# Kernel tuning notes

Hardware: AMD Instinct MI355X
Metric: run time of the kernel (lower is better)

## Reference

```python
import jax, jax.numpy as jnp
import numpy as np

B, T, D = 4, 2048, 1024
H = 16
HD = D // H  # 64
MAX_POS = 4096


def setup_inputs() -> dict:
    key = jax.random.key(0)
    k1, k2, k3, k4 = jax.random.split(key, 4)
    x = jax.random.normal(k1, (B, T, D), dtype=jnp.float32)
    position_ids = jnp.sort(jax.random.randint(k2, (B, T), 0, MAX_POS), axis=-1)
    Wqkv = jax.random.normal(k3, (D, 3 * D), dtype=jnp.float32) * (D ** -0.5)
    Wout = jax.random.normal(k4, (D, D), dtype=jnp.float32) * (D ** -0.5)
    return {"x": x, "position_ids": position_ids, "Wqkv": Wqkv, "Wout": Wout}


def reference(x, position_ids, Wqkv, Wout):
    Bv, Tv, Dv = x.shape
    # qkv projection: (B,T,3,H,HD)
    qkv = (x @ Wqkv).reshape(Bv, Tv, 3, H, HD)
    q, k, v = jnp.moveaxis(qkv, 2, 0)  # each (B,T,H,HD)
    q = q.transpose(0, 2, 1, 3)  # (B,H,T,HD)
    k = k.transpose(0, 2, 1, 3)
    v = v.transpose(0, 2, 1, 3)
    scale = 1.0 / jnp.sqrt(jnp.asarray(HD, dtype=x.dtype))
    attn = jnp.einsum('bhid,bhjd->bhij', q, k) * scale  # (B,H,T,T)
    # position-derived causal mask: attend only where pos_i >= pos_j
    causal_mask = position_ids[:, None, :, None] < position_ids[:, None, None, :]
    attn = jnp.where(causal_mask, -jnp.inf, attn)
    attn = jax.nn.softmax(attn, axis=-1)
    attn = jnp.nan_to_num(attn, nan=0.0)
    out = jnp.einsum('bhij,bhjd->bhid', attn, v)  # (B,H,T,HD)
    out = out.transpose(0, 2, 1, 3).reshape(Bv, Tv, Dv)
    return out @ Wout
```

## Files before the change

### kernel.cpp

```cpp
#include <hip/hip_runtime.h>
#include <math.h>

#define NB 4
#define NT 2048
#define ND 1024
#define NH 16
#define NHD 64
#define N3D 3072
#define M1 8192

typedef __attribute__((ext_vector_type(8))) short bf16x8;
typedef __attribute__((ext_vector_type(4))) float f32x4;
typedef __attribute__((ext_vector_type(16))) float f32x16;
typedef __attribute__((ext_vector_type(2))) int i32x2;
typedef unsigned short u16;
typedef unsigned int u32;

__device__ __forceinline__ u32 bf16rn(float f) {
    u32 u = __float_as_uint(f);
    return (u + 0x7FFFu + ((u >> 16) & 1u)) >> 16;
}
__device__ __forceinline__ u32 pack2(float a, float b) {
    return bf16rn(a) | (bf16rn(b) << 16);
}
__device__ __forceinline__ u32 cvtpk(float lo, float hi) {
    u32 r;
    asm("v_cvt_pk_bf16_f32 %0, %1, %2" : "=v"(r) : "v"(lo), "v"(hi));
    return r;
}
__device__ __forceinline__ void pswap(u32& a, u32& b) {
    i32x2 r = __builtin_amdgcn_permlane32_swap((int)a, (int)b, false, false);
    a = (u32)r.x; b = (u32)r.y;
}

__global__ __launch_bounds__(256) void convx_kernel(const float* __restrict__ in, u16* __restrict__ out) {
    const int idx = blockIdx.x * 256 + threadIdx.x;
    const float4 v = *reinterpret_cast<const float4*>(in + (size_t)idx * 4);
    *reinterpret_cast<uint2*>(out + (size_t)idx * 4) = make_uint2(pack2(v.x, v.y), pack2(v.z, v.w));
}

__global__ __launch_bounds__(256) void tconv_kernel(const float* __restrict__ in, u16* __restrict__ out,
                                                    int R, int C) {
    __shared__ float t[32][33];
    const int bx = blockIdx.x * 32, by = blockIdx.y * 32;
    const int x = threadIdx.x, y0 = threadIdx.y;
    #pragma unroll
    for (int yy = y0; yy < 32; yy += 8) t[yy][x] = in[(size_t)(by + yy) * C + bx + x];
    __syncthreads();
    #pragma unroll
    for (int yy = y0; yy < 32; yy += 8) out[(size_t)(bx + yy) * R + by + x] = (u16)bf16rn(t[x][yy]);
}

#define GEMM_PROLOGUE(Aptr, Btptr)                                                            \
    __shared__ __align__(16) u16 As[4096];                                                    \
    __shared__ __align__(16) u16 Bs[4096];                                                    \
    const int tid = threadIdx.x;                                                              \
    const int lane = tid & 63, wave = tid >> 6;                                               \
    const int wr = wave >> 1, wc = wave & 1;                                                  \
    const int n0 = blockIdx.x * 128, m0 = blockIdx.y * 128;                                   \
    const int c0 = tid, c1 = tid + 256;                                                      \
    const int pA0 = (c0 * 16) ^ ((((c0 * 16) >> 6) & 7) << 4);                                \
    const int pA1 = (c1 * 16) ^ ((((c1 * 16) >> 6) & 7) << 4);                                \
    const u16* gA0 = Aptr + (size_t)(m0 + (c0 >> 2)) * 1024 + (c0 & 3) * 8;                   \
    const u16* gA1 = Aptr + (size_t)(m0 + (c1 >> 2)) * 1024 + (c1 & 3) * 8;                   \
    const u16* gB0 = Btptr + (size_t)(n0 + (c0 >> 2)) * 1024 + (c0 & 3) * 8;                  \
    const u16* gB1 = Btptr + (size_t)(n0 + (c1 >> 2)) * 1024 + (c1 & 3) * 8;                  \
    int offA[4], offB[4];                                                                     \
    {                                                                                         \
        const int kb = (lane >> 4) * 16;                                                      \
        _Pragma("unroll")                                                                     \
        for (int mm = 0; mm < 4; ++mm) {                                                      \
            int row = wr * 64 + mm * 16 + (lane & 15);                                        \
            offA[mm] = (row * 64 + kb) ^ ((row & 7) << 4);                                    \
        }                                                                                     \
        _Pragma("unroll")                                                                     \
        for (int nn = 0; nn < 4; ++nn) {                                                      \
            int row = wc * 64 + nn * 16 + (lane & 15);                                        \
            offB[nn] = (row * 64 + kb) ^ ((row & 7) << 4);                                    \
        }                                                                                     \
    }                                                                                         \
    f32x4 acc[4][4];                                                                          \
    _Pragma("unroll")                                                                         \
    for (int mm = 0; mm < 4; ++mm)                                                            \
        _Pragma("unroll")                                                                     \
        for (int nn = 0; nn < 4; ++nn)                                                        \
            acc[mm][nn] = (f32x4){0.f, 0.f, 0.f, 0.f};                                        \
    uint4 va0 = *(const uint4*)gA0, va1 = *(const uint4*)gA1;                                 \
    uint4 vb0 = *(const uint4*)gB0, vb1 = *(const uint4*)gB1;                                 \
    for (int k0 = 0; k0 < 1024; k0 += 32) {                                                   \
        __syncthreads();                                                                      \
        *(uint4*)((char*)As + pA0) = va0;                                                     \
        *(uint4*)((char*)As + pA1) = va1;                                                     \
        *(uint4*)((char*)Bs + pA0) = vb0;                                                     \
        *(uint4*)((char*)Bs + pA1) = vb1;                                                     \
        __syncthreads();                                                                      \
        if (k0 + 32 < 1024) {                                                                 \
            gA0 += 32; gA1 += 32; gB0 += 32; gB1 += 32;                                       \
            va0 = *(const uint4*)gA0; va1 = *(const uint4*)gA1;                               \
            vb0 = *(const uint4*)gB0; vb1 = *(const uint4*)gB1;                               \
        }                                                                                     \
        bf16x8 aF[4], bF[4];                                                                  \
        _Pragma("unroll")                                                                     \
        for (int mm = 0; mm < 4; ++mm) aF[mm] = *(const bf16x8*)((const char*)As + offA[mm]); \
        _Pragma("unroll")                                                                     \
        for (int nn = 0; nn < 4; ++nn) bF[nn] = *(const bf16x8*)((const char*)Bs + offB[nn]); \
        _Pragma("unroll")                                                                     \
        for (int mm = 0; mm < 4; ++mm)                                                        \
            _Pragma("unroll")                                                                 \
            for (int nn = 0; nn < 4; ++nn)                                                    \
                acc[mm][nn] = __builtin_amdgcn_mfma_f32_16x16x32_bf16(bF[nn], aF[mm],         \
                                                                      acc[mm][nn], 0, 0, 0); \
    }

__global__ __launch_bounds__(256) void gemm_qkv_kernel(
    const u16* __restrict__ A, const u16* __restrict__ Bt,
    u16* __restrict__ Qo, u16* __restrict__ Ko, u16* __restrict__ Vo)
{
    GEMM_PROLOGUE(A, Bt)
    const float qsc = 0.18033688011112042f;
    const int col16 = lane & 15, g4 = (lane >> 4) << 2;
    const int nb0 = n0 + wc * 64;
    const int tb0 = m0 + wr * 64;
    const int s = nb0 >> 10;
    if (s == 0) {
        #pragma unroll
        for (int mm = 0; mm < 4; ++mm) {
            const int t = tb0 + mm * 16 + col16;
            const int bq = t >> 11, tt = t & 2047;
            #pragma unroll
            for (int nn = 0; nn < 4; ++nn) {
                const int n_abs = nb0 + nn * 16 + g4;
                const int hh = (n_abs >> 6) & 15, hd = n_abs & 63;
                uint2 w = make_uint2(pack2(acc[mm][nn][0] * qsc, acc[mm][nn][1] * qsc),
                                     pack2(acc[mm][nn][2] * qsc, acc[mm][nn][3] * qsc));
                *reinterpret_cast<uint2*>(&Qo[((size_t)((bq << 4) + hh) * 2048 + tt) * 64 + hd]) = w;
            }
        }
    } else if (s == 1) {
        #pragma unroll
        for (int mm = 0; mm < 4; ++mm) {
            const int t = tb0 + mm * 16 + col16;
            const int bq = t >> 11, tt = t & 2047;
            #pragma unroll
            for (int nn = 0; nn < 4; ++nn) {
                const int n_abs = nb0 + nn * 16 + g4;
                const int hh = (n_abs >> 6) & 15, hd = n_abs & 63;
                uint2 w = make_uint2(pack2(acc[mm][nn][0], acc[mm][nn][1]),
                                     pack2(acc[mm][nn][2], acc[mm][nn][3]));
                *reinterpret_cast<uint2*>(&Ko[((size_t)((bq << 4) + hh) * 2048 + tt) * 64 + hd]) = w;
            }
        }
    } else {
        #pragma unroll
        for (int mm = 0; mm < 4; ++mm) {
            const int t = tb0 + mm * 16 + col16;
            const int bq = t >> 11, tt = t & 2047;
            #pragma unroll
            for (int nn = 0; nn < 4; ++nn) {
                const int n_abs = nb0 + nn * 16 + g4;
                const int hh = (n_abs >> 6) & 15, hd = n_abs & 63;
                const size_t vbase = ((size_t)((bq << 4) + hh) * 64 + hd) * 2048 + tt;
                #pragma unroll
                for (int r = 0; r < 4; ++r)
                    Vo[vbase + (size_t)r * 2048] = (u16)bf16rn(acc[mm][nn][r]);
            }
        }
    }
}

__global__ __launch_bounds__(256) void gemm_out_kernel(
    const u16* __restrict__ A, const u16* __restrict__ Bt, float* __restrict__ C)
{
    GEMM_PROLOGUE(A, Bt)
    const int col16 = lane & 15, g4 = (lane >> 4) << 2;
    #pragma unroll
    for (int mm = 0; mm < 4; ++mm) {
        const int m = m0 + wr * 64 + mm * 16 + col16;
        #pragma unroll
        for (int nn = 0; nn < 4; ++nn) {
            const int n_a = n0 + wc * 64 + nn * 16 + g4;
            *reinterpret_cast<float4*>(&C[(size_t)m * 1024 + n_a]) =
                make_float4(acc[mm][nn][0], acc[mm][nn][1], acc[mm][nn][2], acc[mm][nn][3]);
        }
    }
}

__global__ __launch_bounds__(64) void attn5_kernel(
    const u16* __restrict__ Q, const u16* __restrict__ K, const u16* __restrict__ Vt,
    const int* __restrict__ pos, u16* __restrict__ AO)
{
    const int bid = blockIdx.x;
    const int wg  = ((bid & 7) << 9) + (bid >> 3);
    const int bh  = wg >> 6;
    const int qw  = 63 - (wg & 63);
    const int b = bh >> 4, h = bh & 15;
    const int lane = threadIdx.x;
    const int col = lane & 31, hi = lane >> 5;
    const int i0 = qw * 32;

    int bnd;
    {
        const int target = pos[b * 2048 + i0 + col];
        int lo = 0, hic = 2048;
        #pragma unroll
        for (int it = 0; it < 12; ++it) {
            const int mid = (lo + hic) >> 1;
            if (lo < hic) { if (pos[b * 2048 + mid] <= target) lo = mid + 1; else hic = mid; }
        }
        bnd = lo;
    }
    int bmax = bnd, bmin = bnd;
    #pragma unroll
    for (int s = 1; s < 32; s <<= 1) {
        bmax = max(bmax, __shfl_xor(bmax, s));
        bmin = min(bmin, __shfl_xor(bmin, s));
    }

    const size_t kvrow = (size_t)bh * 2048;
    const size_t vrow  = (size_t)bh * 64;

    bf16x8 qf[4];
    #pragma unroll
    for (int ds = 0; ds < 4; ++ds)
        qf[ds] = *(const bf16x8*)&Q[(kvrow + i0 + col) * 64 + ds * 16 + hi * 8];

    const int hi4 = 4 * hi;

    float mrun = -INFINITY, lrun = 0.f;
    f32x16 oT0, oT1;
    #pragma unroll
    for (int i = 0; i < 16; ++i) { oT0[i] = 0.f; oT1[i] = 0.f; }

    for (int j0 = 0; j0 < bmax; j0 += 32) {
        bf16x8 kf[4], vfa[2], vfb[2];
        #pragma unroll
        for (int ds = 0; ds < 4; ++ds)
            kf[ds] = *(const bf16x8*)&K[(kvrow + j0 + col) * 64 + ds * 16 + hi * 8];
        #pragma unroll
        for (int kh = 0; kh < 2; ++kh) {
            vfa[kh] = *(const bf16x8*)&Vt[(vrow + col) * 2048 + j0 + kh * 16 + hi * 8];
            vfb[kh] = *(const bf16x8*)&Vt[(vrow + 32 + col) * 2048 + j0 + kh * 16 + hi * 8];
        }

        f32x16 st;
        #pragma unroll
        for (int i = 0; i < 16; ++i) st[i] = 0.f;
        #pragma unroll
        for (int ds = 0; ds < 4; ++ds)
            st = __builtin_amdgcn_mfma_f32_32x32x16_bf16(kf[ds], qf[ds], st, 0, 0, 0);

        if (j0 + 32 > bmin) {
            #pragma unroll
            for (int r = 0; r < 16; ++r) {
                const int kg = j0 + ((r & 3) + 8 * (r >> 2)) + hi4;
                if (kg >= bnd) st[r] = -INFINITY;
            }
        }

        float rm = st[0];
        #pragma unroll
        for (int r = 1; r < 16; ++r) rm = fmaxf(rm, st[r]);
        rm = fmaxf(rm, __shfl_xor(rm, 32));
        if (__any(rm > mrun)) {
            const float mnew = fmaxf(mrun, rm);
            const float factor = __builtin_amdgcn_exp2f(mrun - mnew);
            mrun = mnew;
            lrun *= factor;
            #pragma unroll
            for (int i = 0; i < 16; ++i) { oT0[i] *= factor; oT1[i] *= factor; }
        }
        float psum = 0.f;
        #pragma unroll
        for (int r = 0; r < 16; ++r) {
            const float p = __builtin_amdgcn_exp2f(st[r] - mrun);
            st[r] = p;
            psum += p;
        }
        psum += __shfl_xor(psum, 32);
        lrun += psum;

        u32 W[8];
        #pragma unroll
        for (int r = 0; r < 8; ++r) W[r] = cvtpk(st[2 * r], st[2 * r + 1]);

        u32 a0 = W[0], b0 = W[2]; pswap(a0, b0);
        u32 a1 = W[1], b1 = W[3]; pswap(a1, b1);
        u32 a2 = W[4], b2 = W[6]; pswap(a2, b2);
        u32 a3 = W[5], b3 = W[7]; pswap(a3, b3);
        union { u32 w[4]; bf16x8 v; } p0, p1;
        p0.w[0] = a0; p0.w[1] = a1; p0.w[2] = b0; p0.w[3] = b1;
        p1.w[0] = a2; p1.w[1] = a3; p1.w[2] = b2; p1.w[3] = b3;

        oT0 = __builtin_amdgcn_mfma_f32_32x32x16_bf16(vfa[0], p0.v, oT0, 0, 0, 0);
        oT0 = __builtin_amdgcn_mfma_f32_32x32x16_bf16(vfa[1], p1.v, oT0, 0, 0, 0);
        oT1 = __builtin_amdgcn_mfma_f32_32x32x16_bf16(vfb[0], p0.v, oT1, 0, 0, 0);
        oT1 = __builtin_amdgcn_mfma_f32_32x32x16_bf16(vfb[1], p1.v, oT1, 0, 0, 0);
    }

    const float inv = 1.f / lrun;
    u16* dst = &AO[((size_t)(b * 2048 + i0 + col)) * 1024 + h * 64];
    #pragma unroll
    for (int w = 0; w < 8; ++w) {
        const int dloc = 8 * (w >> 1) + 2 * (w & 1) + hi4;
        *reinterpret_cast<u32*>(&dst[dloc])      = cvtpk(oT0[2 * w] * inv, oT0[2 * w + 1] * inv);
        *reinterpret_cast<u32*>(&dst[32 + dloc]) = cvtpk(oT1[2 * w] * inv, oT1[2 * w + 1] * inv);
    }
}

extern "C" void kernel_launch(void* const* d_in, const int* in_sizes, int n_in,
                              void* d_out, int out_size, void* d_ws, size_t ws_size,
                              hipStream_t stream) {
    (void)in_sizes; (void)n_in; (void)out_size; (void)ws_size;
    const float* x    = (const float*)d_in[0];
    const int*   pos  = (const int*)d_in[1];
    const float* Wqkv = (const float*)d_in[2];
    const float* Wout = (const float*)d_in[3];
    float* out = (float*)d_out;

    char* ws = (char*)d_ws;
    u16* xb    = (u16*)(ws);
    u16* WqkvT = (u16*)(ws + 16777216);
    u16* WoutT = (u16*)(ws + 23068672);
    u16* Qb    = (u16*)(ws + 25165824);
    u16* Kb    = (u16*)(ws + 41943040);
    u16* Vtb   = (u16*)(ws + 58720256);
    u16* AO    = xb;

    convx_kernel<<<dim3(M1 * ND / (256 * 4)), dim3(256), 0, stream>>>(x, xb);
    tconv_kernel<<<dim3(N3D / 32, ND / 32), dim3(32, 8), 0, stream>>>(Wqkv, WqkvT, ND, N3D);
    tconv_kernel<<<dim3(ND / 32, ND / 32), dim3(32, 8), 0, stream>>>(Wout, WoutT, ND, ND);
    gemm_qkv_kernel<<<dim3(N3D / 128, M1 / 128), dim3(256), 0, stream>>>(xb, WqkvT, Qb, Kb, Vtb);
    attn5_kernel<<<dim3(4096), dim3(64), 0, stream>>>(Qb, Kb, Vtb, pos, AO);
    gemm_out_kernel<<<dim3(ND / 128, M1 / 128), dim3(256), 0, stream>>>(AO, WoutT, out);
}
```

Before: 356.6 us.

## Split attention KV range across two workgroups, stage GEMM epilogues through LDS

Attention now runs as a split-K flash-decoding style pass: each 32-query tile is handled by two workgroups covering halves of the key range. Each writes unnormalized bf16 partial outputs plus running max and sum, and a new combine kernel merges them. The causal-boundary binary search moves to a separate precompute kernel. The QKV and output GEMM epilogues now stage tiles through swizzled LDS so global stores are coalesced 16-byte writes, in particular the transposed V layout. The intent is more parallelism and less load imbalance for the long causal rows, and fewer scattered stores, at the cost of an extra partial-buffer round trip, bf16 rounding of the partials, and two more launches.

Measured after the change: 387.2 us. 8.6% more time.

```diff
diff --git a/kernel.cpp b/kernel.cpp
--- a/kernel.cpp
+++ b/kernel.cpp
@@ -16,6 +16,8 @@
 typedef unsigned short u16;
 typedef unsigned int u32;
 
+#define MNEG -3.0e38f
+
 __device__ __forceinline__ u32 bf16rn(float f) {
     u32 u = __float_as_uint(f);
     return (u + 0x7FFFu + ((u >> 16) & 1u)) >> 16;
@@ -31,6 +33,19 @@
 __device__ __forceinline__ void pswap(u32& a, u32& b) {
     i32x2 r = __builtin_amdgcn_permlane32_swap((int)a, (int)b, false, false);
     a = (u32)r.x; b = (u32)r.y;
+}
+
+__global__ __launch_bounds__(256) void bnd_kernel(const int* __restrict__ pos, int* __restrict__ Bnd) {
+    const int row = blockIdx.x * 256 + threadIdx.x;
+    const int b = row >> 11, i = row & 2047;
+    const int target = pos[b * 2048 + i];
+    int lo = 0, hi = 2048;
+    #pragma unroll
+    for (int it = 0; it < 12; ++it) {
+        const int mid = (lo + hi) >> 1;
+        if (lo < hi) { if (pos[b * 2048 + mid] <= target) lo = mid + 1; else hi = mid; }
+    }
+    Bnd[row] = lo;
 }
 
 __global__ __launch_bounds__(256) void convx_kernel(const float* __restrict__ in, u16* __restrict__ out) {
@@ -117,54 +132,63 @@
     u16* __restrict__ Qo, u16* __restrict__ Ko, u16* __restrict__ Vo)
 {
     GEMM_PROLOGUE(A, Bt)
-    const float qsc = 0.18033688011112042f;
     const int col16 = lane & 15, g4 = (lane >> 4) << 2;
     const int nb0 = n0 + wc * 64;
     const int tb0 = m0 + wr * 64;
-    const int s = nb0 >> 10;
-    if (s == 0) {
-        #pragma unroll
-        for (int mm = 0; mm < 4; ++mm) {
-            const int t = tb0 + mm * 16 + col16;
-            const int bq = t >> 11, tt = t & 2047;
-            #pragma unroll
-            for (int nn = 0; nn < 4; ++nn) {
-                const int n_abs = nb0 + nn * 16 + g4;
-                const int hh = (n_abs >> 6) & 15, hd = n_abs & 63;
-                uint2 w = make_uint2(pack2(acc[mm][nn][0] * qsc, acc[mm][nn][1] * qsc),
-                                     pack2(acc[mm][nn][2] * qsc, acc[mm][nn][3] * qsc));
-                *reinterpret_cast<uint2*>(&Qo[((size_t)((bq << 4) + hh) * 2048 + tt) * 64 + hd]) = w;
+    const int s  = nb0 >> 10;
+    const int hh = (nb0 >> 6) & 15;
+    const int t0g = tb0 & 2047;
+    const int bh = ((tb0 >> 11) << 4) + hh;
+    const float sc = (s == 0) ? 0.18033688011112042f : 1.0f;
+
+    __syncthreads();
+    u16* lds = (wave & 1) ? Bs : As;
+    for (int round = 0; round < 2; ++round) {
+        if ((wave >> 1) == round) {
+            if (s < 2) {
+                #pragma unroll
+                for (int mm = 0; mm < 4; ++mm) {
+                    const int tl = mm * 16 + col16;
+                    #pragma unroll
+                    for (int nn = 0; nn < 4; ++nn) {
+                        uint2 w = make_uint2(pack2(acc[mm][nn][0] * sc, acc[mm][nn][1] * sc),
+                                             pack2(acc[mm][nn][2] * sc, acc[mm][nn][3] * sc));
+                        const int off = (tl * 128 + (nn * 16 + g4) * 2) ^ ((tl & 7) << 4);
+                        *reinterpret_cast<uint2*>((char*)lds + off) = w;
+                    }
+                }
+                u16* dst = (s == 0) ? Qo : Ko;
+                #pragma unroll
+                for (int it = 0; it < 8; ++it) {
+                    const int row = it * 8 + (lane >> 3);
+                    const int off = (row * 128 + (lane & 7) * 16) ^ ((row & 7) << 4);
+                    uint4 v = *reinterpret_cast<const uint4*>((const char*)lds + off);
+                    *reinterpret_cast<uint4*>(&dst[((size_t)bh * 2048 + t0g + row) * 64 + (lane & 7) * 8]) = v;
+                }
+            } else {
+                #pragma unroll
+                for (int mm = 0; mm < 4; ++mm) {
+                    const int tl = mm * 16 + col16;
+                    #pragma unroll
+                    for (int nn = 0; nn < 4; ++nn) {
+                        #pragma unroll
+                        for (int r = 0; r < 4; ++r) {
+                            const int dl = nn * 16 + g4 + r;
+                            const int off = (dl * 128 + tl * 2) ^ ((dl & 7) << 4);
+                            *reinterpret_cast<u16*>((char*)lds + off) = (u16)bf16rn(acc[mm][nn][r]);
+                        }
+                    }
+                }
+                #pragma unroll
+                for (int it = 0; it < 8; ++it) {
+                    const int row = it * 8 + (lane >> 3);
+                    const int off = (row * 128 + (lane & 7) * 16) ^ ((row & 7) << 4);
+                    uint4 v = *reinterpret_cast<const uint4*>((const char*)lds + off);
+                    *reinterpret_cast<uint4*>(&Vo[((size_t)bh * 64 + row) * 2048 + t0g + (lane & 7) * 8]) = v;
+                }
             }
         }
-    } else if (s == 1) {
-        #pragma unroll
-        for (int mm = 0; mm < 4; ++mm) {
-            const int t = tb0 + mm * 16 + col16;
-            const int bq = t >> 11, tt = t & 2047;
-            #pragma unroll
-            for (int nn = 0; nn < 4; ++nn) {
-                const int n_abs = nb0 + nn * 16 + g4;
-                const int hh = (n_abs >> 6) & 15, hd = n_abs & 63;
-                uint2 w = make_uint2(pack2(acc[mm][nn][0], acc[mm][nn][1]),
-                                     pack2(acc[mm][nn][2], acc[mm][nn][3]));
-                *reinterpret_cast<uint2*>(&Ko[((size_t)((bq << 4) + hh) * 2048 + tt) * 64 + hd]) = w;
-            }
-        }
-    } else {
-        #pragma unroll
-        for (int mm = 0; mm < 4; ++mm) {
-            const int t = tb0 + mm * 16 + col16;
-            const int bq = t >> 11, tt = t & 2047;
-            #pragma unroll
-            for (int nn = 0; nn < 4; ++nn) {
-                const int n_abs = nb0 + nn * 16 + g4;
-                const int hh = (n_abs >> 6) & 15, hd = n_abs & 63;
-                const size_t vbase = ((size_t)((bq << 4) + hh) * 64 + hd) * 2048 + tt;
-                #pragma unroll
-                for (int r = 0; r < 4; ++r)
-                    Vo[vbase + (size_t)r * 2048] = (u16)bf16rn(acc[mm][nn][r]);
-            }
-        }
+        __syncthreads();
     }
 }
 
@@ -173,48 +197,62 @@
 {
     GEMM_PROLOGUE(A, Bt)
     const int col16 = lane & 15, g4 = (lane >> 4) << 2;
-    #pragma unroll
-    for (int mm = 0; mm < 4; ++mm) {
-        const int m = m0 + wr * 64 + mm * 16 + col16;
-        #pragma unroll
-        for (int nn = 0; nn < 4; ++nn) {
-            const int n_a = n0 + wc * 64 + nn * 16 + g4;
-            *reinterpret_cast<float4*>(&C[(size_t)m * 1024 + n_a]) =
-                make_float4(acc[mm][nn][0], acc[mm][nn][1], acc[mm][nn][2], acc[mm][nn][3]);
-        }
-    }
-}
-
-__global__ __launch_bounds__(64) void attn5_kernel(
+    __syncthreads();
+    char* lds = (char*)((wave & 1) ? Bs : As);
+    for (int round = 0; round < 2; ++round) {
+        if ((wave >> 1) == round) {
+            #pragma unroll
+            for (int p = 0; p < 2; ++p) {
+                #pragma unroll
+                for (int mmh = 0; mmh < 2; ++mmh) {
+                    const int mm = p * 2 + mmh;
+                    const int rl = mmh * 16 + col16;
+                    #pragma unroll
+                    for (int nn = 0; nn < 4; ++nn) {
+                        const int off = (rl * 256 + (nn * 16 + g4) * 4) ^ ((rl & 7) << 4);
+                        *reinterpret_cast<f32x4*>(lds + off) = acc[mm][nn];
+                    }
+                }
+                #pragma unroll
+                for (int it = 0; it < 8; ++it) {
+                    const int row = it * 4 + (lane >> 4);
+                    const int off = (row * 256 + col16 * 16) ^ ((row & 7) << 4);
+                    float4 v = *reinterpret_cast<const float4*>((const char*)lds + off);
+                    const int mg = m0 + wr * 64 + p * 32 + row;
+                    *reinterpret_cast<float4*>(&C[(size_t)mg * 1024 + n0 + wc * 64 + col16 * 4]) = v;
+                }
+            }
+        }
+        __syncthreads();
+    }
+}
+
+__global__ __launch_bounds__(64) void attn6_kernel(
     const u16* __restrict__ Q, const u16* __restrict__ K, const u16* __restrict__ Vt,
-    const int* __restrict__ pos, u16* __restrict__ AO)
+    const int* __restrict__ Bnd, u32* __restrict__ Pout)
 {
     const int bid = blockIdx.x;
-    const int wg  = ((bid & 7) << 9) + (bid >> 3);
-    const int bh  = wg >> 6;
-    const int qw  = 63 - (wg & 63);
-    const int b = bh >> 4, h = bh & 15;
+    const int x = bid & 7, wgl = bid >> 3;
+    const int bh = x * 8 + (wgl >> 7);
+    const int w2 = wgl & 127;
+    const int qi = 63 - (w2 >> 1);
+    const int c  = w2 & 1;
+    const int b = bh >> 4;
     const int lane = threadIdx.x;
-    const int col = lane & 31, hi = lane >> 5;
-    const int i0 = qw * 32;
-
-    int bnd;
-    {
-        const int target = pos[b * 2048 + i0 + col];
-        int lo = 0, hic = 2048;
-        #pragma unroll
-        for (int it = 0; it < 12; ++it) {
-            const int mid = (lo + hic) >> 1;
-            if (lo < hic) { if (pos[b * 2048 + mid] <= target) lo = mid + 1; else hic = mid; }
-        }
-        bnd = lo;
-    }
+    const int col = lane & 31, hi = lane >> 5, hi4 = 4 * hi;
+    const int i0 = qi * 32;
+
+    const int bnd = Bnd[b * 2048 + i0 + col];
     int bmax = bnd, bmin = bnd;
     #pragma unroll
     for (int s = 1; s < 32; s <<= 1) {
         bmax = max(bmax, __shfl_xor(bmax, s));
         bmin = min(bmin, __shfl_xor(bmin, s));
     }
+    const int ntiles = (bmax + 31) >> 5;
+    const int halfk  = ((ntiles + 1) >> 1) << 5;
+    const int kLo = c ? halfk : 0;
+    const int kHi = c ? bmax : min(halfk, bmax);
 
     const size_t kvrow = (size_t)bh * 2048;
     const size_t vrow  = (size_t)bh * 64;
@@ -224,14 +262,12 @@
     for (int ds = 0; ds < 4; ++ds)
         qf[ds] = *(const bf16x8*)&Q[(kvrow + i0 + col) * 64 + ds * 16 + hi * 8];
 
-    const int hi4 = 4 * hi;
-
-    float mrun = -INFINITY, lrun = 0.f;
+    float mrun = MNEG, lrun = 0.f;
     f32x16 oT0, oT1;
     #pragma unroll
     for (int i = 0; i < 16; ++i) { oT0[i] = 0.f; oT1[i] = 0.f; }
 
-    for (int j0 = 0; j0 < bmax; j0 += 32) {
+    for (int j0 = kLo; j0 < kHi; j0 += 32) {
         bf16x8 kf[4], vfa[2], vfb[2];
         #pragma unroll
         for (int ds = 0; ds < 4; ++ds)
@@ -282,7 +318,6 @@
         u32 W[8];
         #pragma unroll
         for (int r = 0; r < 8; ++r) W[r] = cvtpk(st[2 * r], st[2 * r + 1]);
-
         u32 a0 = W[0], b0 = W[2]; pswap(a0, b0);
         u32 a1 = W[1], b1 = W[3]; pswap(a1, b1);
         u32 a2 = W[4], b2 = W[6]; pswap(a2, b2);
@@ -297,13 +332,43 @@
         oT1 = __builtin_amdgcn_mfma_f32_32x32x16_bf16(vfb[1], p1.v, oT1, 0, 0, 0);
     }
 
-    const float inv = 1.f / lrun;
-    u16* dst = &AO[((size_t)(b * 2048 + i0 + col)) * 1024 + h * 64];
-    #pragma unroll
-    for (int w = 0; w < 8; ++w) {
-        const int dloc = 8 * (w >> 1) + 2 * (w & 1) + hi4;
-        *reinterpret_cast<u32*>(&dst[dloc])      = cvtpk(oT0[2 * w] * inv, oT0[2 * w + 1] * inv);
-        *reinterpret_cast<u32*>(&dst[32 + dloc]) = cvtpk(oT1[2 * w] * inv, oT1[2 * w + 1] * inv);
+    const int slot = ((bh << 6) + qi) * 2 + c;
+    u32* P = Pout + (size_t)slot * 1152 + lane;
+    #pragma unroll
+    for (int w = 0; w < 8; ++w) P[w * 64] = cvtpk(oT0[2 * w], oT0[2 * w + 1]);
+    #pragma unroll
+    for (int w = 0; w < 8; ++w) P[(8 + w) * 64] = cvtpk(oT1[2 * w], oT1[2 * w + 1]);
+    P[16 * 64] = __float_as_uint(mrun);
+    P[17 * 64] = __float_as_uint(lrun);
+}
+
+__global__ __launch_bounds__(64) void attn_combine_kernel(
+    const u32* __restrict__ P, u16* __restrict__ AO)
+{
+    const int t = blockIdx.x;
+    const int bh = t >> 6, qi = t & 63;
+    const int b = bh >> 4, h = bh & 15;
+    const int lane = threadIdx.x;
+    const int col = lane & 31, hi4 = 4 * (lane >> 5);
+    const u32* A  = P + (size_t)(t * 2) * 1152 + lane;
+    const u32* Bp = A + 1152;
+    const float mA = __uint_as_float(A[16 * 64]),  lA = __uint_as_float(A[17 * 64]);
+    const float mB = __uint_as_float(Bp[16 * 64]), lB = __uint_as_float(Bp[17 * 64]);
+    const float mN = fmaxf(mA, mB);
+    const float fA = __builtin_amdgcn_exp2f(mA - mN);
+    const float fB = __builtin_amdgcn_exp2f(mB - mN);
+    const float inv = 1.f / (lA * fA + lB * fB);
+    u16* dst = &AO[((size_t)(b * 2048 + qi * 32 + col)) * 1024 + h * 64];
+    #pragma unroll
+    for (int w = 0; w < 16; ++w) {
+        const u32 wa = A[w * 64], wb = Bp[w * 64];
+        const float a0 = __uint_as_float(wa << 16), a1 = __uint_as_float(wa & 0xFFFF0000u);
+        const float b0 = __uint_as_float(wb << 16), b1 = __uint_as_float(wb & 0xFFFF0000u);
+        const float o0 = (a0 * fA + b0 * fB) * inv;
+        const float o1 = (a1 * fA + b1 * fB) * inv;
+        const int wl = w & 7;
+        const int dloc = 8 * (wl >> 1) + 2 * (wl & 1) + hi4 + ((w >> 3) << 5);
+        *reinterpret_cast<u32*>(&dst[dloc]) = cvtpk(o0, o1);
     }
 }
 
@@ -324,12 +389,16 @@
     u16* Qb    = (u16*)(ws + 25165824);
     u16* Kb    = (u16*)(ws + 41943040);
     u16* Vtb   = (u16*)(ws + 58720256);
+    u32* Part  = (u32*)(ws + 75497472);
+    int* Bnd   = (int*)(ws + 113246208);
     u16* AO    = xb;
 
+    bnd_kernel<<<dim3(M1 / 256), dim3(256), 0, stream>>>(pos, Bnd);
     convx_kernel<<<dim3(M1 * ND / (256 * 4)), dim3(256), 0, stream>>>(x, xb);
     tconv_kernel<<<dim3(N3D / 32, ND / 32), dim3(32, 8), 0, stream>>>(Wqkv, WqkvT, ND, N3D);
     tconv_kernel<<<dim3(ND / 32, ND / 32), dim3(32, 8), 0, stream>>>(Wout, WoutT, ND, ND);
     gemm_qkv_kernel<<<dim3(N3D / 128, M1 / 128), dim3(256), 0, stream>>>(xb, WqkvT, Qb, Kb, Vtb);
-    attn5_kernel<<<dim3(4096), dim3(64), 0, stream>>>(Qb, Kb, Vtb, pos, AO);
+    attn6_kernel<<<dim3(8192), dim3(64), 0, stream>>>(Qb, Kb, Vtb, Bnd, Part);
+    attn_combine_kernel<<<dim3(4096), dim3(64), 0, stream>>>(Part, AO);
     gemm_out_kernel<<<dim3(ND / 128, M1 / 128), dim3(256), 0, stream>>>(AO, WoutT, out);
 }
```
